# Performance work log

Measured on AMD Instinct MI355X. Metric: run time of the kernel, lower is better.

## Reference

```python
import jax, jax.numpy as jnp
import numpy as np

POOL_H, POOL_W = 7, 7


def _crop_and_resize(fmap, boxes, box_idx, ph, pw):
    """TF tf.image.crop_and_resize (bilinear) for normalized boxes.
    fmap: [B,H,W,C], boxes: [M,4] (y1,x1,y2,x2), box_idx: [M] int32 -> [M,ph,pw,C]."""
    H, W = fmap.shape[1], fmap.shape[2]
    dt = fmap.dtype
    y1, x1, y2, x2 = jnp.split(boxes.astype(dt), 4, axis=1)  # each [M,1]
    gy = jnp.arange(ph, dtype=dt) / (ph - 1)
    gx = jnp.arange(pw, dtype=dt) / (pw - 1)
    ys = (y1 + (y2 - y1) * gy[None, :]) * (H - 1)  # [M,ph]
    xs = (x1 + (x2 - x1) * gx[None, :]) * (W - 1)  # [M,pw]
    y0 = jnp.clip(jnp.floor(ys), 0, H - 1).astype(jnp.int32)
    x0 = jnp.clip(jnp.floor(xs), 0, W - 1).astype(jnp.int32)
    y1i = jnp.minimum(y0 + 1, H - 1)
    x1i = jnp.minimum(x0 + 1, W - 1)
    ly = (ys - y0.astype(dt))[:, :, None, None]  # [M,ph,1,1]
    lx = (xs - x0.astype(dt))[:, None, :, None]  # [M,1,pw,1]
    b = box_idx[:, None, None]
    tl = fmap[b, y0[:, :, None], x0[:, None, :]]   # [M,ph,pw,C]
    tr = fmap[b, y0[:, :, None], x1i[:, None, :]]
    bl = fmap[b, y1i[:, :, None], x0[:, None, :]]
    br = fmap[b, y1i[:, :, None], x1i[:, None, :]]
    top = tl + (tr - tl) * lx
    bot = bl + (br - bl) * lx
    return top + (bot - top) * ly


def pyramid_roi_align(boxes, image_meta, feature_maps):
    B, N, _ = boxes.shape
    y1, x1, y2, x2 = jnp.split(boxes, 4, axis=2)
    h = y2 - y1
    w = x2 - x1
    image_shape = image_meta[0, 4:7]
    image_area = image_shape[0] * image_shape[1]
    roi_level = jnp.log2(jnp.sqrt(h * w) / (224.0 / jnp.sqrt(image_area)))
    roi_level = jnp.clip(4 + jnp.round(roi_level).astype(jnp.int32), 2, 5)
    roi_level = roi_level.reshape(B * N)  # squeeze axis 2 + flatten

    flat_boxes = boxes.reshape(B * N, 4)
    box_idx = jnp.repeat(jnp.arange(B, dtype=jnp.int32), N)
    C = feature_maps[0].shape[-1]
    pooled = jnp.zeros((B * N, POOL_H, POOL_W, C), dtype=feature_maps[0].dtype)
    # Equivalent to TF's gather/crop/sort-restore: each box pooled from its level.
    for i, level in enumerate(range(2, 6)):
        crop = _crop_and_resize(feature_maps[i], flat_boxes, box_idx, POOL_H, POOL_W)
        mask = (roi_level == level)[:, None, None, None]
        pooled = jnp.where(mask, crop, pooled)
    return pooled.reshape(B, N, POOL_H, POOL_W, C)


def setup_inputs() -> dict:
    key = jax.random.key(0)
    k1, k2, k3, k4, k5, k6, k7, k8 = jax.random.split(key, 8)
    B, N, C = 2, 1000, 256
    # boxes: normalized y1,x1,y2,x2 with sizes spanning all FPN levels
    sz = jax.random.uniform(k1, (B, N, 1), minval=0.02, maxval=0.8)
    yx1 = jax.random.uniform(k2, (B, N, 2)) * (1.0 - sz)
    boxes = jnp.concatenate([yx1[..., :1], yx1[..., 1:], yx1[..., :1] + sz, yx1[..., 1:] + sz], axis=2)
    # image_meta: image_shape (1024,1024,3) at indices 4:7
    meta = np.zeros((B, 93), dtype=np.float32)
    meta[:, 1:4] = [1024, 1024, 3]
    meta[:, 4:7] = [1024, 1024, 3]
    meta[:, 11] = 1.0
    return {
        "boxes": boxes.astype(jnp.float32),
        "image_meta": jnp.asarray(meta),
        "feat_p2": jax.random.normal(k3, (B, 256, 256, C), dtype=jnp.float32),
        "feat_p3": jax.random.normal(k4, (B, 128, 128, C), dtype=jnp.float32),
        "feat_p4": jax.random.normal(k5, (B, 64, 64, C), dtype=jnp.float32),
        "feat_p5": jax.random.normal(k6, (B, 32, 32, C), dtype=jnp.float32),
    }


def reference(boxes, image_meta, feat_p2, feat_p3, feat_p4, feat_p5):
    return pyramid_roi_align(boxes, image_meta, (feat_p2, feat_p3, feat_p4, feat_p5))
```

## Files before the change

### kernel.cpp

```cpp
#include <hip/hip_runtime.h>
#include <math.h>


#define POOLN 7
#define CCH 256

typedef float f32x4 __attribute__((ext_vector_type(4)));

struct __align__(16) AxisInfo { int r0; int r1; float l; int pad; };

__global__ __launch_bounds__(64) void roi_prep_kernel(
    const float* __restrict__ boxes,
    const float* __restrict__ meta,
    int* __restrict__ liArr,
    AxisInfo* __restrict__ yinfo,
    AxisInfo* __restrict__ xinfo,
    int n_boxes, int boxes_per_batch)
{
    int tid = blockIdx.x * blockDim.x + threadIdx.x;
    int box = tid / POOLN;
    int j   = tid - box * POOLN;
    if (box >= n_boxes) return;

    float by1 = boxes[4 * box + 0];
    float bx1 = boxes[4 * box + 1];
    float by2 = boxes[4 * box + 2];
    float bx2 = boxes[4 * box + 3];
    float h = by2 - by1, w = bx2 - bx1;

    float area  = meta[4] * meta[5];
    float scale = 224.0f / sqrtf(area);
    float rl    = log2f(sqrtf(h * w) / scale);
    int lvl = 4 + (int)rintf(rl);
    lvl = lvl < 2 ? 2 : (lvl > 5 ? 5 : lvl);
    int li = lvl - 2;
    int H  = 256 >> li;
    if (j == 0) liArr[box] = li;

    int b = box / boxes_per_batch;
    float g = (float)j / 6.0f;
    float hm1 = (float)(H - 1);

    float ys  = (by1 + h * g) * hm1;
    float fy0 = fminf(fmaxf(floorf(ys), 0.0f), hm1);
    int y0  = (int)fy0;
    int y1i = min(y0 + 1, H - 1);
    AxisInfo yi;
    yi.r0 = ((b * H + y0)  * H) * CCH;
    yi.r1 = ((b * H + y1i) * H) * CCH;
    yi.l  = ys - fy0;
    yi.pad = 0;
    yinfo[box * POOLN + j] = yi;

    float xs  = (bx1 + w * g) * hm1;
    float fx0 = fminf(fmaxf(floorf(xs), 0.0f), hm1);
    int x0  = (int)fx0;
    int x1i = min(x0 + 1, H - 1);
    AxisInfo xi;
    xi.r0 = x0  * CCH;
    xi.r1 = x1i * CCH;
    xi.l  = xs - fx0;
    xi.pad = 0;
    xinfo[box * POOLN + j] = xi;
}

__device__ __forceinline__ f32x4 bilerp4(f32x4 tl, f32x4 tr, f32x4 bl, f32x4 br,
                                         float lx, float ly)
{
    f32x4 r;
    float top, bot;
    top = tl.x + (tr.x - tl.x) * lx; bot = bl.x + (br.x - bl.x) * lx; r.x = top + (bot - top) * ly;
    top = tl.y + (tr.y - tl.y) * lx; bot = bl.y + (br.y - bl.y) * lx; r.y = top + (bot - top) * ly;
    top = tl.z + (tr.z - tl.z) * lx; bot = bl.z + (br.z - bl.z) * lx; r.z = top + (bot - top) * ly;
    top = tl.w + (tr.w - tl.w) * lx; bot = bl.w + (br.w - bl.w) * lx; r.w = top + (bot - top) * ly;
    return r;
}

__global__ __launch_bounds__(256) void roi_gather_kernel(
    const int* __restrict__ liArr,
    const AxisInfo* __restrict__ yinfo,
    const AxisInfo* __restrict__ xinfo,
    const float* __restrict__ f2,
    const float* __restrict__ f3,
    const float* __restrict__ f4,
    const float* __restrict__ f5,
    float* __restrict__ out,
    int q, int r, long total)
{
    int bid    = blockIdx.x;
    int xcd    = bid & 7;
    int within = bid >> 3;
    int wg = (xcd < r ? xcd * (q + 1) : r * (q + 1) + (xcd - r) * q) + within;

    long wid = (long)wg * 256 + threadIdx.x;
    if (wid >= total) return;

    int  c4  = (int)(wid & 31);
    long t   = wid >> 5;
    int  box = (int)(t / 49);
    int  p   = (int)(t - (long)box * 49);
    int  py  = (p * 37) >> 8;
    int  px  = p - py * 7;

    int li = liArr[box];
    const float* f = (li == 0) ? f2 : (li == 1) ? f3 : (li == 2) ? f4 : f5;
    AxisInfo yi = yinfo[box * POOLN + py];
    AxisInfo xi = xinfo[box * POOLN + px];
    float ly = yi.l, lx = xi.l;

    int co = c4 * 4;
    const float* ptl = f + yi.r0 + xi.r0 + co;
    const float* ptr2= f + yi.r0 + xi.r1 + co;
    const float* pbl = f + yi.r1 + xi.r0 + co;
    const float* pbr = f + yi.r1 + xi.r1 + co;

    f32x4 tlA = *(const f32x4*)ptl;
    f32x4 trA = *(const f32x4*)ptr2;
    f32x4 blA = *(const f32x4*)pbl;
    f32x4 brA = *(const f32x4*)pbr;
    f32x4 tlB = *(const f32x4*)(ptl + 128);
    f32x4 trB = *(const f32x4*)(ptr2 + 128);
    f32x4 blB = *(const f32x4*)(pbl + 128);
    f32x4 brB = *(const f32x4*)(pbr + 128);

    f32x4 rA = bilerp4(tlA, trA, blA, brA, lx, ly);
    f32x4 rB = bilerp4(tlB, trB, blB, brB, lx, ly);

    long obase = t * CCH + co;
    __builtin_nontemporal_store(rA, (f32x4*)(out + obase));
    __builtin_nontemporal_store(rB, (f32x4*)(out + obase + 128));
}

__global__ __launch_bounds__(256) void roi_align_kernel(
    const float* __restrict__ boxes,
    const float* __restrict__ meta,
    const float* __restrict__ f2,
    const float* __restrict__ f3,
    const float* __restrict__ f4,
    const float* __restrict__ f5,
    float* __restrict__ out,
    int boxes_per_batch,
    long total4)
{
    long idx = (long)blockIdx.x * blockDim.x + threadIdx.x;
    if (idx >= total4) return;

    int c4  = (int)(idx & 63);
    long t  = idx >> 6;
    int p   = (int)(t % 49);
    int box = (int)(t / 49);
    int py = p / 7, px = p % 7;

    float by1 = boxes[4 * box + 0];
    float bx1 = boxes[4 * box + 1];
    float by2 = boxes[4 * box + 2];
    float bx2 = boxes[4 * box + 3];

    float h = by2 - by1, w = bx2 - bx1;
    float area  = meta[4] * meta[5];
    float scale = 224.0f / sqrtf(area);
    float rl    = log2f(sqrtf(h * w) / scale);
    int lvl = 4 + (int)rintf(rl);
    lvl = lvl < 2 ? 2 : (lvl > 5 ? 5 : lvl);
    int li = lvl - 2;
    const float* f = (li == 0) ? f2 : (li == 1) ? f3 : (li == 2) ? f4 : f5;
    int H = 256 >> li;

    int b = box / boxes_per_batch;

    float gy = (float)py / 6.0f;
    float gx = (float)px / 6.0f;
    float ys = (by1 + (by2 - by1) * gy) * (float)(H - 1);
    float xs = (bx1 + (bx2 - bx1) * gx) * (float)(H - 1);

    float fy0 = fminf(fmaxf(floorf(ys), 0.0f), (float)(H - 1));
    float fx0 = fminf(fmaxf(floorf(xs), 0.0f), (float)(H - 1));
    int y0 = (int)fy0, x0 = (int)fx0;
    int y1i = min(y0 + 1, H - 1);
    int x1i = min(x0 + 1, H - 1);
    float ly = ys - fy0;
    float lx = xs - fx0;

    size_t row0 = ((size_t)b * H + y0)  * H;
    size_t row1 = ((size_t)b * H + y1i) * H;
    const f32x4* tl = (const f32x4*)(f + (row0 + x0)  * CCH) + c4;
    const f32x4* tr = (const f32x4*)(f + (row0 + x1i) * CCH) + c4;
    const f32x4* bl = (const f32x4*)(f + (row1 + x0)  * CCH) + c4;
    const f32x4* br = (const f32x4*)(f + (row1 + x1i) * CCH) + c4;

    f32x4 rr = bilerp4(*tl, *tr, *bl, *br, lx, ly);
    ((f32x4*)out)[idx] = rr;
}

extern "C" void kernel_launch(void* const* d_in, const int* in_sizes, int n_in,
                              void* d_out, int out_size, void* d_ws, size_t ws_size,
                              hipStream_t stream) {
    const float* boxes = (const float*)d_in[0];
    const float* meta  = (const float*)d_in[1];
    const float* f2    = (const float*)d_in[2];
    const float* f3    = (const float*)d_in[3];
    const float* f4    = (const float*)d_in[4];
    const float* f5    = (const float*)d_in[5];
    float* out         = (float*)d_out;

    int n_boxes = in_sizes[0] / 4;
    int B       = in_sizes[2] / (256 * 256 * 256);
    int boxes_per_batch = n_boxes / B;

    size_t li_bytes   = 16384;
    size_t axis_bytes = (size_t)n_boxes * POOLN * sizeof(AxisInfo);
    size_t need = li_bytes + 2 * axis_bytes;

    if (d_ws != nullptr && ws_size >= need) {
        int*      liArr = (int*)d_ws;
        AxisInfo* yinfo = (AxisInfo*)((char*)d_ws + li_bytes);
        AxisInfo* xinfo = yinfo + (size_t)n_boxes * POOLN;

        int prep_threads = n_boxes * POOLN;
        roi_prep_kernel<<<(prep_threads + 63) / 64, 64, 0, stream>>>(
            boxes, meta, liArr, yinfo, xinfo, n_boxes, boxes_per_batch);

        long total = (long)n_boxes * 49 * 32;
        int  nwg   = (int)((total + 255) / 256);
        int  q = nwg >> 3, r = nwg & 7;
        roi_gather_kernel<<<nwg, 256, 0, stream>>>(
            liArr, yinfo, xinfo, f2, f3, f4, f5, out, q, r, total);
    } else {
        long total4 = (long)n_boxes * 49 * 64;
        int  blocks = (int)((total4 + 255) / 256);
        roi_align_kernel<<<blocks, 256, 0, stream>>>(
            boxes, meta, f2, f3, f4, f5, out, boxes_per_batch, total4);
    }
}
```

Before: 42.40 us.

## Precompute per-pixel gather records and widen per-thread channel work

The prep kernel now emits one 32-byte record per output pixel, holding the four corner offsets, both weights and the pyramid level, in place of separate per-axis tables plus a level array. The gather kernel loads one record instead of three lookups and drops the divide-by-49 index math. Each thread now handles 16 contiguous channels (four float4 per corner) instead of two strided halves, which halves the thread count. Output stores become regular stores instead of nontemporal. This trades more prep-kernel work and workspace traffic for less per-thread index arithmetic and more memory-level parallelism per thread, at the cost of higher register pressure and fewer wavefronts in flight.

Result: slower. 71.51 us (+68.7%).

```diff
diff --git a/kernel.cpp b/kernel.cpp
--- a/kernel.cpp
+++ b/kernel.cpp
@@ -6,21 +6,28 @@
 #define CCH 256
 
 typedef float f32x4 __attribute__((ext_vector_type(4)));
-
-struct __align__(16) AxisInfo { int r0; int r1; float l; int pad; };
-
-__global__ __launch_bounds__(64) void roi_prep_kernel(
+typedef int   i32x4 __attribute__((ext_vector_type(4)));
+
+struct __align__(16) PixRec {
+    int   tl, tr, bl, br;
+    float lx, ly;
+    int   li, pad;
+};
+
+__global__ __launch_bounds__(256) void roi_prep_kernel(
     const float* __restrict__ boxes,
     const float* __restrict__ meta,
-    int* __restrict__ liArr,
-    AxisInfo* __restrict__ yinfo,
-    AxisInfo* __restrict__ xinfo,
+    PixRec* __restrict__ recs,
     int n_boxes, int boxes_per_batch)
 {
-    int tid = blockIdx.x * blockDim.x + threadIdx.x;
-    int box = tid / POOLN;
-    int j   = tid - box * POOLN;
-    if (box >= n_boxes) return;
+    int t = blockIdx.x * blockDim.x + threadIdx.x;
+    int total = n_boxes * 49;
+    if (t >= total) return;
+
+    int box = t / 49;
+    int p   = t - box * 49;
+    int py  = (p * 37) >> 8;
+    int px  = p - py * 7;
 
     float by1 = boxes[4 * box + 0];
     float bx1 = boxes[4 * box + 1];
@@ -35,33 +42,34 @@
     lvl = lvl < 2 ? 2 : (lvl > 5 ? 5 : lvl);
     int li = lvl - 2;
     int H  = 256 >> li;
-    if (j == 0) liArr[box] = li;
-
+    float hm1 = (float)(H - 1);
     int b = box / boxes_per_batch;
-    float g = (float)j / 6.0f;
-    float hm1 = (float)(H - 1);
-
-    float ys  = (by1 + h * g) * hm1;
+
+    float gy  = (float)py / 6.0f;
+    float ys  = (by1 + h * gy) * hm1;
     float fy0 = fminf(fmaxf(floorf(ys), 0.0f), hm1);
     int y0  = (int)fy0;
     int y1i = min(y0 + 1, H - 1);
-    AxisInfo yi;
-    yi.r0 = ((b * H + y0)  * H) * CCH;
-    yi.r1 = ((b * H + y1i) * H) * CCH;
-    yi.l  = ys - fy0;
-    yi.pad = 0;
-    yinfo[box * POOLN + j] = yi;
-
-    float xs  = (bx1 + w * g) * hm1;
+
+    float gx  = (float)px / 6.0f;
+    float xs  = (bx1 + w * gx) * hm1;
     float fx0 = fminf(fmaxf(floorf(xs), 0.0f), hm1);
     int x0  = (int)fx0;
     int x1i = min(x0 + 1, H - 1);
-    AxisInfo xi;
-    xi.r0 = x0  * CCH;
-    xi.r1 = x1i * CCH;
-    xi.l  = xs - fx0;
-    xi.pad = 0;
-    xinfo[box * POOLN + j] = xi;
+
+    int row0 = (b * H + y0)  * H;
+    int row1 = (b * H + y1i) * H;
+
+    PixRec r;
+    r.tl = (row0 + x0)  * CCH;
+    r.tr = (row0 + x1i) * CCH;
+    r.bl = (row1 + x0)  * CCH;
+    r.br = (row1 + x1i) * CCH;
+    r.lx = xs - fx0;
+    r.ly = ys - fy0;
+    r.li = li;
+    r.pad = 0;
+    recs[t] = r;
 }
 
 __device__ __forceinline__ f32x4 bilerp4(f32x4 tl, f32x4 tr, f32x4 bl, f32x4 br,
@@ -77,9 +85,7 @@
 }
 
 __global__ __launch_bounds__(256) void roi_gather_kernel(
-    const int* __restrict__ liArr,
-    const AxisInfo* __restrict__ yinfo,
-    const AxisInfo* __restrict__ xinfo,
+    const PixRec* __restrict__ recs,
     const float* __restrict__ f2,
     const float* __restrict__ f3,
     const float* __restrict__ f4,
@@ -95,40 +101,31 @@
     long wid = (long)wg * 256 + threadIdx.x;
     if (wid >= total) return;
 
-    int  c4  = (int)(wid & 31);
-    long t   = wid >> 5;
-    int  box = (int)(t / 49);
-    int  p   = (int)(t - (long)box * 49);
-    int  py  = (p * 37) >> 8;
-    int  px  = p - py * 7;
-
-    int li = liArr[box];
-    const float* f = (li == 0) ? f2 : (li == 1) ? f3 : (li == 2) ? f4 : f5;
-    AxisInfo yi = yinfo[box * POOLN + py];
-    AxisInfo xi = xinfo[box * POOLN + px];
-    float ly = yi.l, lx = xi.l;
-
-    int co = c4 * 4;
-    const float* ptl = f + yi.r0 + xi.r0 + co;
-    const float* ptr2= f + yi.r0 + xi.r1 + co;
-    const float* pbl = f + yi.r1 + xi.r0 + co;
-    const float* pbr = f + yi.r1 + xi.r1 + co;
-
-    f32x4 tlA = *(const f32x4*)ptl;
-    f32x4 trA = *(const f32x4*)ptr2;
-    f32x4 blA = *(const f32x4*)pbl;
-    f32x4 brA = *(const f32x4*)pbr;
-    f32x4 tlB = *(const f32x4*)(ptl + 128);
-    f32x4 trB = *(const f32x4*)(ptr2 + 128);
-    f32x4 blB = *(const f32x4*)(pbl + 128);
-    f32x4 brB = *(const f32x4*)(pbr + 128);
-
-    f32x4 rA = bilerp4(tlA, trA, blA, brA, lx, ly);
-    f32x4 rB = bilerp4(tlB, trB, blB, brB, lx, ly);
-
-    long obase = t * CCH + co;
-    __builtin_nontemporal_store(rA, (f32x4*)(out + obase));
-    __builtin_nontemporal_store(rB, (f32x4*)(out + obase + 128));
+    int  c16 = (int)(wid & 15);
+    long t   = wid >> 4;
+
+    PixRec rec = recs[t];
+    const float* f = (rec.li == 0) ? f2 : (rec.li == 1) ? f3 : (rec.li == 2) ? f4 : f5;
+    float lx = rec.lx, ly = rec.ly;
+
+    int co = c16 * 16;
+    const f32x4* ptl = (const f32x4*)(f + rec.tl + co);
+    const f32x4* ptr2= (const f32x4*)(f + rec.tr + co);
+    const f32x4* pbl = (const f32x4*)(f + rec.bl + co);
+    const f32x4* pbr = (const f32x4*)(f + rec.br + co);
+
+    f32x4 tl0 = ptl[0], tl1 = ptl[1], tl2 = ptl[2], tl3 = ptl[3];
+    f32x4 tr0 = ptr2[0], tr1 = ptr2[1], tr2 = ptr2[2], tr3 = ptr2[3];
+    f32x4 bl0 = pbl[0], bl1 = pbl[1], bl2 = pbl[2], bl3 = pbl[3];
+    f32x4 br0 = pbr[0], br1 = pbr[1], br2 = pbr[2], br3 = pbr[3];
+
+    f32x4 r0 = bilerp4(tl0, tr0, bl0, br0, lx, ly);
+    f32x4 r1 = bilerp4(tl1, tr1, bl1, br1, lx, ly);
+    f32x4 r2 = bilerp4(tl2, tr2, bl2, br2, lx, ly);
+    f32x4 r3 = bilerp4(tl3, tr3, bl3, br3, lx, ly);
+
+    f32x4* po = (f32x4*)(out + t * CCH + co);
+    po[0] = r0; po[1] = r1; po[2] = r2; po[3] = r3;
 }
 
 __global__ __launch_bounds__(256) void roi_align_kernel(
@@ -207,24 +204,20 @@
     int B       = in_sizes[2] / (256 * 256 * 256);
     int boxes_per_batch = n_boxes / B;
 
-    size_t li_bytes   = 16384;
-    size_t axis_bytes = (size_t)n_boxes * POOLN * sizeof(AxisInfo);
-    size_t need = li_bytes + 2 * axis_bytes;
+    int    n_pix = n_boxes * 49;
+    size_t need  = (size_t)n_pix * sizeof(PixRec);
 
     if (d_ws != nullptr && ws_size >= need) {
-        int*      liArr = (int*)d_ws;
-        AxisInfo* yinfo = (AxisInfo*)((char*)d_ws + li_bytes);
-        AxisInfo* xinfo = yinfo + (size_t)n_boxes * POOLN;
-
-        int prep_threads = n_boxes * POOLN;
-        roi_prep_kernel<<<(prep_threads + 63) / 64, 64, 0, stream>>>(
-            boxes, meta, liArr, yinfo, xinfo, n_boxes, boxes_per_batch);
-
-        long total = (long)n_boxes * 49 * 32;
+        PixRec* recs = (PixRec*)d_ws;
+
+        roi_prep_kernel<<<(n_pix + 255) / 256, 256, 0, stream>>>(
+            boxes, meta, recs, n_boxes, boxes_per_batch);
+
+        long total = (long)n_pix * 16;
         int  nwg   = (int)((total + 255) / 256);
         int  q = nwg >> 3, r = nwg & 7;
         roi_gather_kernel<<<nwg, 256, 0, stream>>>(
-            liArr, yinfo, xinfo, f2, f3, f4, f5, out, q, r, total);
+            recs, f2, f3, f4, f5, out, q, r, total);
     } else {
         long total4 = (long)n_boxes * 49 * 64;
         int  blocks = (int)((total4 + 255) / 256);
```
